# Kernel optimization log

Hardware: AMD Instinct MI355X
Metric: run time of the kernel (lower is better)

The kernel has to match this reference:

```python
import jax, jax.numpy as jnp
import numpy as np

B, C, L = 4, 192, 4096
DIV = 3
CO = C // DIV  # 64


def setup_inputs() -> dict:
    key = jax.random.key(0)
    ks = jax.random.split(key, 6)
    # kaiming-normal-ish init for 1x1 conv weights, stored as (out, in) matrices
    std = float(np.sqrt(2.0 / C))
    return {
        "x": jax.random.normal(ks[0], (B, C, L, 1), dtype=jnp.float32),
        "Wq": jax.random.normal(ks[1], (CO, C), dtype=jnp.float32) * std,
        "Wk": jax.random.normal(ks[2], (CO, C), dtype=jnp.float32) * std,
        "Wv": jax.random.normal(ks[3], (CO, C), dtype=jnp.float32) * std,
        "Wv1": jax.random.normal(ks[4], (CO, C), dtype=jnp.float32) * std,
        "gamma": jnp.zeros((1,), dtype=jnp.float32) + 0.5,  # nonzero so attn path is exercised
    }


def reference(x, Wq, Wk, Wv, Wv1, gamma):
    b, c, l, _ = x.shape
    xf = x.reshape(b, c, l)                      # (B, C, L)
    f = jnp.einsum("oc,bcl->bol", Wq, xf)        # (B, CO, L)
    g = jnp.einsum("oc,bcl->bol", Wk, xf)
    h = jnp.einsum("oc,bcl->bol", Wv, xf)
    v1 = jnp.einsum("oc,bcl->bol", Wv1, xf)
    # scores[b, l, m] = sum_o f[b,o,l] * g[b,o,m]; softmax over dim=1 (l axis)
    scores = jnp.einsum("bol,bom->blm", f, g)    # (B, L, L)
    beta = jax.nn.softmax(scores, axis=1)
    o = gamma * jnp.einsum("bol,blm->bom", h, beta) + v1  # (B, CO, L)
    return o.reshape(b, c // 3, l, 1)
```

## Files before the change

### kernel.cpp

```cpp
#include <hip/hip_runtime.h>
#include <math.h>

#define B_ 4
#define C_ 192
#define L_ 4096
#define CO_ 64
#define LOG2E 1.44269504088896340736f

using half8 = __attribute__((ext_vector_type(8))) _Float16;
using half4v = __attribute__((ext_vector_type(4))) _Float16;
using half2v = __attribute__((ext_vector_type(2))) _Float16;
using f32x16 = __attribute__((ext_vector_type(16))) float;

#if __has_builtin(__builtin_amdgcn_exp2f)
#define EXP2(x) __builtin_amdgcn_exp2f(x)
#else
#define EXP2(x) exp2f(x)
#endif

__device__ inline half2v pkrtz(float a, float b) {
  return __builtin_bit_cast(half2v, __builtin_amdgcn_cvt_pkrtz(a, b));
}


__global__ __launch_bounds__(256) void wpack_kernel(
    const float* __restrict__ Wq, const float* __restrict__ Wk,
    const float* __restrict__ Wv, const float* __restrict__ Wv1,
    _Float16* __restrict__ Wpack) {
  const int tid = blockIdx.x * 256 + threadIdx.x;
  const int w = tid / 1536;
  const int rem = tid % 1536;
  const int og = rem / 768;
  const int ks = (rem % 768) / 64;
  const int lane = rem % 64;
  const float* src = (w == 0) ? Wq : (w == 1) ? Wk : (w == 2) ? Wv : Wv1;
  const float s = (w == 0) ? LOG2E : 1.0f;
  const int row = og * 32 + (lane & 31);
  const int col = ks * 16 + (lane >> 5) * 8;
  const float* p = src + row * C_ + col;
  const float4 a = *(const float4*)(p);
  const float4 c = *(const float4*)(p + 4);
  half8 o;
  half2v t;
  t = pkrtz(a.x * s, a.y * s); o[0] = t[0]; o[1] = t[1];
  t = pkrtz(a.z * s, a.w * s); o[2] = t[0]; o[3] = t[1];
  t = pkrtz(c.x * s, c.y * s); o[4] = t[0]; o[5] = t[1];
  t = pkrtz(c.z * s, c.w * s); o[6] = t[0]; o[7] = t[1];
  *(half8*)(Wpack + (size_t)tid * 8) = o;
}

__global__ __launch_bounds__(256) void proj_mfma(
    const float* __restrict__ x, const _Float16* __restrict__ Wpack,
    _Float16* __restrict__ fPack, _Float16* __restrict__ gPack,
    _Float16* __restrict__ hPack, float* __restrict__ v1N) {
  __shared__ __align__(16) _Float16 xT[32][200];
  __shared__ __align__(16) _Float16 fl[32 * 72];
  __shared__ __align__(16) _Float16 gl[32 * 72];
  __shared__ __align__(16) _Float16 hl[64 * 40];
  __shared__ float vl[64][33];
  const int b = blockIdx.y, T = blockIdx.x, l0 = T * 32;
  const int t = threadIdx.x;
  const int lane = t & 63, w = t >> 6;
  const int m = lane & 31, hi = lane >> 5;
  const int lr = lane & 31, rp = lane >> 5;

  const _Float16* Wp = Wpack + (size_t)w * 1536 * 8;
  half8 wf[2][12];
#pragma unroll
  for (int og = 0; og < 2; ++og)
#pragma unroll
    for (int ks = 0; ks < 12; ++ks)
      wf[og][ks] =
          *(const half8*)(Wp + ((size_t)(og * 12 + ks) * 64 + lane) * 8);

  {
    const float* xb = x + (size_t)b * C_ * L_ + l0 + lr;
    const int c0 = w * 48;
#pragma unroll
    for (int i = 0; i < 24; ++i) {
      const int c = c0 + 2 * i + rp;
      xT[lr][c] = (_Float16)xb[(size_t)c * L_];
    }
  }
  __syncthreads();

  half8 aF[12];
#pragma unroll
  for (int ks = 0; ks < 12; ++ks)
    aF[ks] = *(const half8*)&xT[m][ks * 16 + hi * 8];

  f32x16 acc0 = {}, acc1 = {};
#pragma unroll
  for (int ks = 0; ks < 12; ++ks) {
    acc0 = __builtin_amdgcn_mfma_f32_32x32x16_f16(aF[ks], wf[0][ks], acc0, 0, 0, 0);
    acc1 = __builtin_amdgcn_mfma_f32_32x32x16_f16(aF[ks], wf[1][ks], acc1, 0, 0, 0);
  }

  if (w < 2) {
    _Float16* buf = (w == 0) ? fl : gl;
#pragma unroll
    for (int r = 0; r < 16; ++r) {
      const int l = 4 * hi + 8 * (r >> 2) + (r & 3);
      buf[l * 72 + m] = (_Float16)acc0[r];
      buf[l * 72 + 32 + m] = (_Float16)acc1[r];
    }
    _Float16* dst = ((w == 0) ? fPack : gPack) +
                    (size_t)b * L_ * CO_ + (size_t)T * 4 * 64 * 8;
#pragma unroll
    for (int ks = 0; ks < 4; ++ks) {
      const half8 v =
          *(const half8*)&buf[(lane & 31) * 72 + ks * 16 + (lane >> 5) * 8];
      *(half8*)(dst + ((size_t)ks * 64 + lane) * 8) = v;
    }
  } else if (w == 2) {
#pragma unroll
    for (int r = 0; r < 16; ++r) {
      const int l = 4 * hi + 8 * (r >> 2) + (r & 3);
      hl[m * 40 + l] = (_Float16)acc0[r];
      hl[(32 + m) * 40 + l] = (_Float16)acc1[r];
    }
    _Float16* dst = hPack + (size_t)b * L_ * CO_ + (size_t)T * 4 * 64 * 8;
#pragma unroll
    for (int j = 0; j < 4; ++j) {
      const int oh2 = j >> 1, ks2 = j & 1;
      const half8 v = *(const half8*)&hl[(32 * oh2 + (lane & 31)) * 40 +
                                         ks2 * 16 + (lane >> 5) * 8];
      *(half8*)(dst + ((size_t)j * 64 + lane) * 8) = v;
    }
  } else {
#pragma unroll
    for (int r = 0; r < 16; ++r) {
      const int l = 4 * hi + 8 * (r >> 2) + (r & 3);
      vl[m][l] = acc0[r];
      vl[32 + m][l] = acc1[r];
    }
#pragma unroll
    for (int i = 0; i < 32; ++i) {
      const int o = 2 * i + rp;
      v1N[((size_t)b * CO_ + o) * L_ + l0 + lr] = vl[o][lr];
    }
  }
}

__global__ __launch_bounds__(512, 2) void attn_mfma(
    const _Float16* __restrict__ fPack, const _Float16* __restrict__ gPack,
    const _Float16* __restrict__ hPack, const float* __restrict__ v1N,
    const float* __restrict__ gamma_p, float* __restrict__ out) {
  __shared__ __align__(16) _Float16 Pl[8][64 * 40];
  __shared__ float obuf4[4][CO_][65];
  __shared__ float redM[8][64];
  __shared__ float redZ[8][64];

  const int id = blockIdx.x;
  const int b = (id >> 1) & 3;
  const int mt = ((id & 1) << 5) | (id >> 3);
  const int m0 = mt * 64;
  const int t = threadIdx.x;
  const int lane = t & 63, s = t >> 6;
  const int m = lane & 31, hi = lane >> 5;

  const _Float16* fT = fPack + (size_t)b * L_ * CO_;
  const _Float16* hT = hPack + (size_t)b * L_ * CO_;
  _Float16* Pw = &Pl[s][0];

  half8 gf0[4], gf1[4];
  {
    const _Float16* gp = gPack + (size_t)b * L_ * CO_ +
                         (size_t)(2 * mt) * 4 * 64 * 8 + lane * 8;
#pragma unroll
    for (int ks = 0; ks < 4; ++ks) {
      gf0[ks] = *(const half8*)(gp + (size_t)ks * 64 * 8);
      gf1[ks] = *(const half8*)(gp + (size_t)(4 + ks) * 64 * 8);
    }
  }

  f32x16 o0 = {}, o1 = {}, o2 = {}, o3 = {};
  float mx0 = -1e30f, Z0 = 0.f, mx1 = -1e30f, Z1 = 0.f;

  const int T0 = s * 16;
  half8 fc[2][4];
  f32x16 Sv0[2], Sv1[2];

  {
    const _Float16* fp = fT + ((size_t)T0 * 4 * 64 + lane) * 8;
#pragma unroll
    for (int ks = 0; ks < 4; ++ks)
      fc[0][ks] = *(const half8*)(fp + (size_t)ks * 64 * 8);
    f32x16 z = {};
    Sv0[0] = z; Sv1[0] = z;
#pragma unroll
    for (int ks = 0; ks < 4; ++ks) {
      Sv0[0] = __builtin_amdgcn_mfma_f32_32x32x16_f16(fc[0][ks], gf0[ks], Sv0[0], 0, 0, 0);
      Sv1[0] = __builtin_amdgcn_mfma_f32_32x32x16_f16(fc[0][ks], gf1[ks], Sv1[0], 0, 0, 0);
    }
    const _Float16* fp1 = fT + ((size_t)(T0 + 1) * 4 * 64 + lane) * 8;
#pragma unroll
    for (int ks = 0; ks < 4; ++ks)
      fc[1][ks] = *(const half8*)(fp1 + (size_t)ks * 64 * 8);
  }

#pragma unroll 2
  for (int stp = 0; stp < 16; ++stp) {
    const int cur = stp & 1, nxt = cur ^ 1;
    half8 hc[4];
    {
      const _Float16* hp = hT + ((size_t)(T0 + stp) * 4 * 64 + lane) * 8;
#pragma unroll
      for (int ks = 0; ks < 4; ++ks)
        hc[ks] = *(const half8*)(hp + (size_t)ks * 64 * 8);
    }
    {
      f32x16 z = {};
      Sv0[nxt] = z; Sv1[nxt] = z;
#pragma unroll
      for (int ks = 0; ks < 4; ++ks) {
        Sv0[nxt] = __builtin_amdgcn_mfma_f32_32x32x16_f16(fc[nxt][ks], gf0[ks], Sv0[nxt], 0, 0, 0);
        Sv1[nxt] = __builtin_amdgcn_mfma_f32_32x32x16_f16(fc[nxt][ks], gf1[ks], Sv1[nxt], 0, 0, 0);
      }
    }
    {
      const _Float16* fp = fT + ((size_t)(T0 + stp + 2) * 4 * 64 + lane) * 8;
#pragma unroll
      for (int ks = 0; ks < 4; ++ks)
        fc[cur][ks] = *(const half8*)(fp + (size_t)ks * 64 * 8);
    }
    const f32x16 S0 = Sv0[cur], S1 = Sv1[cur];
    float t0 = S0[0], t1 = S1[0];
#pragma unroll
    for (int r = 1; r < 16; ++r) {
      t0 = fmaxf(t0, S0[r]);
      t1 = fmaxf(t1, S1[r]);
    }
    t0 = fmaxf(t0, __shfl_xor(t0, 32, 64));
    t1 = fmaxf(t1, __shfl_xor(t1, 32, 64));
    if (__any(t0 > mx0 || t1 > mx1)) {
      const float mn0 = fmaxf(mx0, t0), mn1 = fmaxf(mx1, t1);
      const float c0 = EXP2(mx0 - mn0), c1 = EXP2(mx1 - mn1);
      mx0 = mn0; mx1 = mn1;
      Z0 *= c0; Z1 *= c1;
#pragma unroll
      for (int r = 0; r < 16; ++r) {
        o0[r] *= c0; o1[r] *= c0;
        o2[r] *= c1; o3[r] *= c1;
      }
    }
    float zl0 = 0.f, zl1 = 0.f;
#pragma unroll
    for (int u = 0; u < 4; ++u) {
      const float a0 = EXP2(S0[4 * u + 0] - mx0);
      const float a1 = EXP2(S0[4 * u + 1] - mx0);
      const float a2 = EXP2(S0[4 * u + 2] - mx0);
      const float a3 = EXP2(S0[4 * u + 3] - mx0);
      zl0 += (a0 + a1) + (a2 + a3);
      const half2v lo = pkrtz(a0, a1);
      const half2v hi2 = pkrtz(a2, a3);
      half4v w4; w4[0] = lo[0]; w4[1] = lo[1]; w4[2] = hi2[0]; w4[3] = hi2[1];
      *(half4v*)(Pw + m * 40 + 4 * hi + 8 * u) = w4;
      const float b0 = EXP2(S1[4 * u + 0] - mx1);
      const float b1 = EXP2(S1[4 * u + 1] - mx1);
      const float b2 = EXP2(S1[4 * u + 2] - mx1);
      const float b3 = EXP2(S1[4 * u + 3] - mx1);
      zl1 += (b0 + b1) + (b2 + b3);
      const half2v lo2 = pkrtz(b0, b1);
      const half2v hi3 = pkrtz(b2, b3);
      half4v w5; w5[0] = lo2[0]; w5[1] = lo2[1]; w5[2] = hi3[0]; w5[3] = hi3[1];
      *(half4v*)(Pw + (32 + m) * 40 + 4 * hi + 8 * u) = w5;
    }
    Z0 += zl0; Z1 += zl1;
    const half8 bP0 = *(const half8*)(Pw + m * 40 + 8 * hi);
    const half8 bP1 = *(const half8*)(Pw + m * 40 + 16 + 8 * hi);
    const half8 bQ0 = *(const half8*)(Pw + (32 + m) * 40 + 8 * hi);
    const half8 bQ1 = *(const half8*)(Pw + (32 + m) * 40 + 16 + 8 * hi);
    o0 = __builtin_amdgcn_mfma_f32_32x32x16_f16(hc[0], bP0, o0, 0, 0, 0);
    o1 = __builtin_amdgcn_mfma_f32_32x32x16_f16(hc[2], bP0, o1, 0, 0, 0);
    o2 = __builtin_amdgcn_mfma_f32_32x32x16_f16(hc[0], bQ0, o2, 0, 0, 0);
    o3 = __builtin_amdgcn_mfma_f32_32x32x16_f16(hc[2], bQ0, o3, 0, 0, 0);
    o0 = __builtin_amdgcn_mfma_f32_32x32x16_f16(hc[1], bP1, o0, 0, 0, 0);
    o1 = __builtin_amdgcn_mfma_f32_32x32x16_f16(hc[3], bP1, o1, 0, 0, 0);
    o2 = __builtin_amdgcn_mfma_f32_32x32x16_f16(hc[1], bQ1, o2, 0, 0, 0);
    o3 = __builtin_amdgcn_mfma_f32_32x32x16_f16(hc[3], bQ1, o3, 0, 0, 0);
  }

  Z0 += __shfl_xor(Z0, 32, 64);
  Z1 += __shfl_xor(Z1, 32, 64);
  if (hi == 0) {
    redM[s][m] = mx0; redM[s][m + 32] = mx1;
    redZ[s][m] = Z0;  redZ[s][m + 32] = Z1;
  }
  __syncthreads();
  float M0 = redM[0][m], M1 = redM[0][m + 32];
#pragma unroll
  for (int i = 1; i < 8; ++i) {
    M0 = fmaxf(M0, redM[i][m]);
    M1 = fmaxf(M1, redM[i][m + 32]);
  }
  const float sc0 = EXP2(mx0 - M0);
  const float sc1 = EXP2(mx1 - M1);
  if (s < 4) {
#pragma unroll
    for (int r = 0; r < 16; ++r) {
      const int o = 4 * hi + 8 * (r >> 2) + (r & 3);
      obuf4[s][o][m] = sc0 * o0[r];
      obuf4[s][o + 32][m] = sc0 * o1[r];
      obuf4[s][o][m + 32] = sc1 * o2[r];
      obuf4[s][o + 32][m + 32] = sc1 * o3[r];
    }
  }
  __syncthreads();
  if (s >= 4) {
#pragma unroll
    for (int r = 0; r < 16; ++r) {
      const int o = 4 * hi + 8 * (r >> 2) + (r & 3);
      obuf4[s - 4][o][m] += sc0 * o0[r];
      obuf4[s - 4][o + 32][m] += sc0 * o1[r];
      obuf4[s - 4][o][m + 32] += sc1 * o2[r];
      obuf4[s - 4][o + 32][m + 32] += sc1 * o3[r];
    }
  }
  __syncthreads();

  const float gam = gamma_p[0];
  const int me = t & 63;
  const int og = t >> 6;
  float M = redM[0][me];
#pragma unroll
  for (int i = 1; i < 8; ++i) M = fmaxf(M, redM[i][me]);
  float Zt = 0.f;
#pragma unroll
  for (int i = 0; i < 8; ++i) Zt += EXP2(redM[i][me] - M) * redZ[i][me];
  const float inv = 1.0f / Zt;
#pragma unroll
  for (int i = 0; i < 8; ++i) {
    const int o = og * 8 + i;
    const float val = obuf4[0][o][me] + obuf4[1][o][me] +
                      obuf4[2][o][me] + obuf4[3][o][me];
    const size_t g = ((size_t)b * CO_ + o) * L_ + m0 + me;
    out[g] = gam * val * inv + v1N[g];
  }
}

extern "C" void kernel_launch(void* const* d_in, const int* in_sizes, int n_in,
                              void* d_out, int out_size, void* d_ws,
                              size_t ws_size, hipStream_t stream) {
  const float* x = (const float*)d_in[0];
  const float* Wq = (const float*)d_in[1];
  const float* Wk = (const float*)d_in[2];
  const float* Wv = (const float*)d_in[3];
  const float* Wv1 = (const float*)d_in[4];
  const float* gamma = (const float*)d_in[5];
  float* out = (float*)d_out;

  _Float16* Wpack = (_Float16*)d_ws;
  _Float16* fPack = Wpack + (size_t)4 * 1536 * 8;
  _Float16* gPack = fPack + (size_t)B_ * L_ * CO_;
  _Float16* hPack = gPack + (size_t)B_ * L_ * CO_;
  float* v1N = (float*)(hPack + (size_t)B_ * L_ * CO_);

  wpack_kernel<<<24, 256, 0, stream>>>(Wq, Wk, Wv, Wv1, Wpack);
  proj_mfma<<<dim3(L_ / 32, B_), 256, 0, stream>>>(x, Wpack, fPack, gPack,
                                                   hPack, v1N);
  attn_mfma<<<256, 512, 0, stream>>>(fPack, gPack, hPack, v1N, gamma, out);
}
```

Before: 105.1 us.

## Compute softmax denominator via MFMA with ones and restructure f/h prefetch

After: 107.4 us. 1.02x slower.

```diff
diff --git a/kernel.cpp b/kernel.cpp
--- a/kernel.cpp
+++ b/kernel.cpp
@@ -174,57 +174,45 @@
     }
   }
 
+  half8 ones8;
+#pragma unroll
+  for (int e = 0; e < 8; ++e) ones8[e] = (_Float16)1.0f;
+
   f32x16 o0 = {}, o1 = {}, o2 = {}, o3 = {};
-  float mx0 = -1e30f, Z0 = 0.f, mx1 = -1e30f, Z1 = 0.f;
+  f32x16 oz0 = {}, oz1 = {};
+  float mx0 = -1e30f, mx1 = -1e30f;
 
   const int T0 = s * 16;
-  half8 fc[2][4];
-  f32x16 Sv0[2], Sv1[2];
-
+  half8 fc[2][4], hc[2][4];
   {
     const _Float16* fp = fT + ((size_t)T0 * 4 * 64 + lane) * 8;
-#pragma unroll
-    for (int ks = 0; ks < 4; ++ks)
+    const _Float16* hp = hT + ((size_t)T0 * 4 * 64 + lane) * 8;
+#pragma unroll
+    for (int ks = 0; ks < 4; ++ks) {
       fc[0][ks] = *(const half8*)(fp + (size_t)ks * 64 * 8);
-    f32x16 z = {};
-    Sv0[0] = z; Sv1[0] = z;
-#pragma unroll
-    for (int ks = 0; ks < 4; ++ks) {
-      Sv0[0] = __builtin_amdgcn_mfma_f32_32x32x16_f16(fc[0][ks], gf0[ks], Sv0[0], 0, 0, 0);
-      Sv1[0] = __builtin_amdgcn_mfma_f32_32x32x16_f16(fc[0][ks], gf1[ks], Sv1[0], 0, 0, 0);
-    }
-    const _Float16* fp1 = fT + ((size_t)(T0 + 1) * 4 * 64 + lane) * 8;
-#pragma unroll
-    for (int ks = 0; ks < 4; ++ks)
-      fc[1][ks] = *(const half8*)(fp1 + (size_t)ks * 64 * 8);
+      hc[0][ks] = *(const half8*)(hp + (size_t)ks * 64 * 8);
+    }
   }
 
 #pragma unroll 2
   for (int stp = 0; stp < 16; ++stp) {
     const int cur = stp & 1, nxt = cur ^ 1;
-    half8 hc[4];
     {
-      const _Float16* hp = hT + ((size_t)(T0 + stp) * 4 * 64 + lane) * 8;
-#pragma unroll
-      for (int ks = 0; ks < 4; ++ks)
-        hc[ks] = *(const half8*)(hp + (size_t)ks * 64 * 8);
-    }
-    {
-      f32x16 z = {};
-      Sv0[nxt] = z; Sv1[nxt] = z;
+      const int Tn = T0 + stp + 1;
+      const _Float16* fp = fT + ((size_t)Tn * 4 * 64 + lane) * 8;
+      const _Float16* hp = hT + ((size_t)Tn * 4 * 64 + lane) * 8;
 #pragma unroll
       for (int ks = 0; ks < 4; ++ks) {
-        Sv0[nxt] = __builtin_amdgcn_mfma_f32_32x32x16_f16(fc[nxt][ks], gf0[ks], Sv0[nxt], 0, 0, 0);
-        Sv1[nxt] = __builtin_amdgcn_mfma_f32_32x32x16_f16(fc[nxt][ks], gf1[ks], Sv1[nxt], 0, 0, 0);
+        fc[nxt][ks] = *(const half8*)(fp + (size_t)ks * 64 * 8);
+        hc[nxt][ks] = *(const half8*)(hp + (size_t)ks * 64 * 8);
       }
     }
-    {
-      const _Float16* fp = fT + ((size_t)(T0 + stp + 2) * 4 * 64 + lane) * 8;
-#pragma unroll
-      for (int ks = 0; ks < 4; ++ks)
-        fc[cur][ks] = *(const half8*)(fp + (size_t)ks * 64 * 8);
-    }
-    const f32x16 S0 = Sv0[cur], S1 = Sv1[cur];
+    f32x16 S0 = {}, S1 = {};
+#pragma unroll
+    for (int ks = 0; ks < 4; ++ks) {
+      S0 = __builtin_amdgcn_mfma_f32_32x32x16_f16(fc[cur][ks], gf0[ks], S0, 0, 0, 0);
+      S1 = __builtin_amdgcn_mfma_f32_32x32x16_f16(fc[cur][ks], gf1[ks], S1, 0, 0, 0);
+    }
     float t0 = S0[0], t1 = S1[0];
 #pragma unroll
     for (int r = 1; r < 16; ++r) {
@@ -237,21 +225,18 @@
       const float mn0 = fmaxf(mx0, t0), mn1 = fmaxf(mx1, t1);
       const float c0 = EXP2(mx0 - mn0), c1 = EXP2(mx1 - mn1);
       mx0 = mn0; mx1 = mn1;
-      Z0 *= c0; Z1 *= c1;
 #pragma unroll
       for (int r = 0; r < 16; ++r) {
-        o0[r] *= c0; o1[r] *= c0;
-        o2[r] *= c1; o3[r] *= c1;
+        o0[r] *= c0; o1[r] *= c0; oz0[r] *= c0;
+        o2[r] *= c1; o3[r] *= c1; oz1[r] *= c1;
       }
     }
-    float zl0 = 0.f, zl1 = 0.f;
 #pragma unroll
     for (int u = 0; u < 4; ++u) {
       const float a0 = EXP2(S0[4 * u + 0] - mx0);
       const float a1 = EXP2(S0[4 * u + 1] - mx0);
       const float a2 = EXP2(S0[4 * u + 2] - mx0);
       const float a3 = EXP2(S0[4 * u + 3] - mx0);
-      zl0 += (a0 + a1) + (a2 + a3);
       const half2v lo = pkrtz(a0, a1);
       const half2v hi2 = pkrtz(a2, a3);
       half4v w4; w4[0] = lo[0]; w4[1] = lo[1]; w4[2] = hi2[0]; w4[3] = hi2[1];
@@ -260,29 +245,31 @@
       const float b1 = EXP2(S1[4 * u + 1] - mx1);
       const float b2 = EXP2(S1[4 * u + 2] - mx1);
       const float b3 = EXP2(S1[4 * u + 3] - mx1);
-      zl1 += (b0 + b1) + (b2 + b3);
       const half2v lo2 = pkrtz(b0, b1);
       const half2v hi3 = pkrtz(b2, b3);
       half4v w5; w5[0] = lo2[0]; w5[1] = lo2[1]; w5[2] = hi3[0]; w5[3] = hi3[1];
       *(half4v*)(Pw + (32 + m) * 40 + 4 * hi + 8 * u) = w5;
     }
-    Z0 += zl0; Z1 += zl1;
     const half8 bP0 = *(const half8*)(Pw + m * 40 + 8 * hi);
     const half8 bP1 = *(const half8*)(Pw + m * 40 + 16 + 8 * hi);
     const half8 bQ0 = *(const half8*)(Pw + (32 + m) * 40 + 8 * hi);
     const half8 bQ1 = *(const half8*)(Pw + (32 + m) * 40 + 16 + 8 * hi);
-    o0 = __builtin_amdgcn_mfma_f32_32x32x16_f16(hc[0], bP0, o0, 0, 0, 0);
-    o1 = __builtin_amdgcn_mfma_f32_32x32x16_f16(hc[2], bP0, o1, 0, 0, 0);
-    o2 = __builtin_amdgcn_mfma_f32_32x32x16_f16(hc[0], bQ0, o2, 0, 0, 0);
-    o3 = __builtin_amdgcn_mfma_f32_32x32x16_f16(hc[2], bQ0, o3, 0, 0, 0);
-    o0 = __builtin_amdgcn_mfma_f32_32x32x16_f16(hc[1], bP1, o0, 0, 0, 0);
-    o1 = __builtin_amdgcn_mfma_f32_32x32x16_f16(hc[3], bP1, o1, 0, 0, 0);
-    o2 = __builtin_amdgcn_mfma_f32_32x32x16_f16(hc[1], bQ1, o2, 0, 0, 0);
-    o3 = __builtin_amdgcn_mfma_f32_32x32x16_f16(hc[3], bQ1, o3, 0, 0, 0);
-  }
-
-  Z0 += __shfl_xor(Z0, 32, 64);
-  Z1 += __shfl_xor(Z1, 32, 64);
+    o0 = __builtin_amdgcn_mfma_f32_32x32x16_f16(hc[cur][0], bP0, o0, 0, 0, 0);
+    o1 = __builtin_amdgcn_mfma_f32_32x32x16_f16(hc[cur][2], bP0, o1, 0, 0, 0);
+    o2 = __builtin_amdgcn_mfma_f32_32x32x16_f16(hc[cur][0], bQ0, o2, 0, 0, 0);
+    o3 = __builtin_amdgcn_mfma_f32_32x32x16_f16(hc[cur][2], bQ0, o3, 0, 0, 0);
+    oz0 = __builtin_amdgcn_mfma_f32_32x32x16_f16(ones8, bP0, oz0, 0, 0, 0);
+    oz1 = __builtin_amdgcn_mfma_f32_32x32x16_f16(ones8, bQ0, oz1, 0, 0, 0);
+    o0 = __builtin_amdgcn_mfma_f32_32x32x16_f16(hc[cur][1], bP1, o0, 0, 0, 0);
+    o1 = __builtin_amdgcn_mfma_f32_32x32x16_f16(hc[cur][3], bP1, o1, 0, 0, 0);
+    o2 = __builtin_amdgcn_mfma_f32_32x32x16_f16(hc[cur][1], bQ1, o2, 0, 0, 0);
+    o3 = __builtin_amdgcn_mfma_f32_32x32x16_f16(hc[cur][3], bQ1, o3, 0, 0, 0);
+    oz0 = __builtin_amdgcn_mfma_f32_32x32x16_f16(ones8, bP1, oz0, 0, 0, 0);
+    oz1 = __builtin_amdgcn_mfma_f32_32x32x16_f16(ones8, bQ1, oz1, 0, 0, 0);
+  }
+
+  const float Z0 = oz0[0];
+  const float Z1 = oz1[0];
   if (hi == 0) {
     redM[s][m] = mx0; redM[s][m + 32] = mx1;
     redZ[s][m] = Z0;  redZ[s][m + 32] = Z1;
```

## Double attention block waves to 16 and shrink per-wave P buffer

Applied to the files above, without the earlier changes.

Measured after the change: 142.1 us. 1.35x slower.

```diff
diff --git a/kernel.cpp b/kernel.cpp
--- a/kernel.cpp
+++ b/kernel.cpp
@@ -142,14 +142,15 @@
   }
 }
 
-__global__ __launch_bounds__(512, 2) void attn_mfma(
+__global__ __launch_bounds__(1024, 4) void attn_mfma(
     const _Float16* __restrict__ fPack, const _Float16* __restrict__ gPack,
     const _Float16* __restrict__ hPack, const float* __restrict__ v1N,
     const float* __restrict__ gamma_p, float* __restrict__ out) {
-  __shared__ __align__(16) _Float16 Pl[8][64 * 40];
-  __shared__ float obuf4[4][CO_][65];
-  __shared__ float redM[8][64];
-  __shared__ float redZ[8][64];
+  __shared__ __align__(16) char smemRaw[4 * 64 * 65 * 4];
+  __shared__ float redM[16][64];
+  __shared__ float redZ[16][64];
+  _Float16* Pall = (_Float16*)smemRaw;
+  float(*obuf4)[CO_][65] = (float(*)[CO_][65])smemRaw;
 
   const int id = blockIdx.x;
   const int b = (id >> 1) & 3;
@@ -161,7 +162,7 @@
 
   const _Float16* fT = fPack + (size_t)b * L_ * CO_;
   const _Float16* hT = hPack + (size_t)b * L_ * CO_;
-  _Float16* Pw = &Pl[s][0];
+  _Float16* Pw = Pall + s * 32 * 40;
 
   half8 gf0[4], gf1[4];
   {
@@ -177,54 +178,21 @@
   f32x16 o0 = {}, o1 = {}, o2 = {}, o3 = {};
   float mx0 = -1e30f, Z0 = 0.f, mx1 = -1e30f, Z1 = 0.f;
 
-  const int T0 = s * 16;
-  half8 fc[2][4];
-  f32x16 Sv0[2], Sv1[2];
-
-  {
-    const _Float16* fp = fT + ((size_t)T0 * 4 * 64 + lane) * 8;
-#pragma unroll
-    for (int ks = 0; ks < 4; ++ks)
-      fc[0][ks] = *(const half8*)(fp + (size_t)ks * 64 * 8);
-    f32x16 z = {};
-    Sv0[0] = z; Sv1[0] = z;
+  for (int stp = 0; stp < 8; ++stp) {
+    const int Tn = s * 8 + stp;
+    half8 fc[4];
+    {
+      const _Float16* fp = fT + ((size_t)Tn * 4 * 64 + lane) * 8;
+#pragma unroll
+      for (int ks = 0; ks < 4; ++ks)
+        fc[ks] = *(const half8*)(fp + (size_t)ks * 64 * 8);
+    }
+    f32x16 S0 = {}, S1 = {};
 #pragma unroll
     for (int ks = 0; ks < 4; ++ks) {
-      Sv0[0] = __builtin_amdgcn_mfma_f32_32x32x16_f16(fc[0][ks], gf0[ks], Sv0[0], 0, 0, 0);
-      Sv1[0] = __builtin_amdgcn_mfma_f32_32x32x16_f16(fc[0][ks], gf1[ks], Sv1[0], 0, 0, 0);
-    }
-    const _Float16* fp1 = fT + ((size_t)(T0 + 1) * 4 * 64 + lane) * 8;
-#pragma unroll
-    for (int ks = 0; ks < 4; ++ks)
-      fc[1][ks] = *(const half8*)(fp1 + (size_t)ks * 64 * 8);
-  }
-
-#pragma unroll 2
-  for (int stp = 0; stp < 16; ++stp) {
-    const int cur = stp & 1, nxt = cur ^ 1;
-    half8 hc[4];
-    {
-      const _Float16* hp = hT + ((size_t)(T0 + stp) * 4 * 64 + lane) * 8;
-#pragma unroll
-      for (int ks = 0; ks < 4; ++ks)
-        hc[ks] = *(const half8*)(hp + (size_t)ks * 64 * 8);
-    }
-    {
-      f32x16 z = {};
-      Sv0[nxt] = z; Sv1[nxt] = z;
-#pragma unroll
-      for (int ks = 0; ks < 4; ++ks) {
-        Sv0[nxt] = __builtin_amdgcn_mfma_f32_32x32x16_f16(fc[nxt][ks], gf0[ks], Sv0[nxt], 0, 0, 0);
-        Sv1[nxt] = __builtin_amdgcn_mfma_f32_32x32x16_f16(fc[nxt][ks], gf1[ks], Sv1[nxt], 0, 0, 0);
-      }
-    }
-    {
-      const _Float16* fp = fT + ((size_t)(T0 + stp + 2) * 4 * 64 + lane) * 8;
-#pragma unroll
-      for (int ks = 0; ks < 4; ++ks)
-        fc[cur][ks] = *(const half8*)(fp + (size_t)ks * 64 * 8);
-    }
-    const f32x16 S0 = Sv0[cur], S1 = Sv1[cur];
+      S0 = __builtin_amdgcn_mfma_f32_32x32x16_f16(fc[ks], gf0[ks], S0, 0, 0, 0);
+      S1 = __builtin_amdgcn_mfma_f32_32x32x16_f16(fc[ks], gf1[ks], S1, 0, 0, 0);
+    }
     float t0 = S0[0], t1 = S1[0];
 #pragma unroll
     for (int r = 1; r < 16; ++r) {
@@ -234,9 +202,9 @@
     t0 = fmaxf(t0, __shfl_xor(t0, 32, 64));
     t1 = fmaxf(t1, __shfl_xor(t1, 32, 64));
     if (__any(t0 > mx0 || t1 > mx1)) {
-      const float mn0 = fmaxf(mx0, t0), mn1 = fmaxf(mx1, t1);
-      const float c0 = EXP2(mx0 - mn0), c1 = EXP2(mx1 - mn1);
-      mx0 = mn0; mx1 = mn1;
+      const float c0 = EXP2(mx0 - fmaxf(mx0, t0));
+      const float c1 = EXP2(mx1 - fmaxf(mx1, t1));
+      mx0 = fmaxf(mx0, t0); mx1 = fmaxf(mx1, t1);
       Z0 *= c0; Z1 *= c1;
 #pragma unroll
       for (int r = 0; r < 16; ++r) {
@@ -244,41 +212,57 @@
         o2[r] *= c1; o3[r] *= c1;
       }
     }
-    float zl0 = 0.f, zl1 = 0.f;
-#pragma unroll
-    for (int u = 0; u < 4; ++u) {
-      const float a0 = EXP2(S0[4 * u + 0] - mx0);
-      const float a1 = EXP2(S0[4 * u + 1] - mx0);
-      const float a2 = EXP2(S0[4 * u + 2] - mx0);
-      const float a3 = EXP2(S0[4 * u + 3] - mx0);
-      zl0 += (a0 + a1) + (a2 + a3);
-      const half2v lo = pkrtz(a0, a1);
-      const half2v hi2 = pkrtz(a2, a3);
-      half4v w4; w4[0] = lo[0]; w4[1] = lo[1]; w4[2] = hi2[0]; w4[3] = hi2[1];
-      *(half4v*)(Pw + m * 40 + 4 * hi + 8 * u) = w4;
-      const float b0 = EXP2(S1[4 * u + 0] - mx1);
-      const float b1 = EXP2(S1[4 * u + 1] - mx1);
-      const float b2 = EXP2(S1[4 * u + 2] - mx1);
-      const float b3 = EXP2(S1[4 * u + 3] - mx1);
-      zl1 += (b0 + b1) + (b2 + b3);
-      const half2v lo2 = pkrtz(b0, b1);
-      const half2v hi3 = pkrtz(b2, b3);
-      half4v w5; w5[0] = lo2[0]; w5[1] = lo2[1]; w5[2] = hi3[0]; w5[3] = hi3[1];
-      *(half4v*)(Pw + (32 + m) * 40 + 4 * hi + 8 * u) = w5;
-    }
-    Z0 += zl0; Z1 += zl1;
-    const half8 bP0 = *(const half8*)(Pw + m * 40 + 8 * hi);
-    const half8 bP1 = *(const half8*)(Pw + m * 40 + 16 + 8 * hi);
-    const half8 bQ0 = *(const half8*)(Pw + (32 + m) * 40 + 8 * hi);
-    const half8 bQ1 = *(const half8*)(Pw + (32 + m) * 40 + 16 + 8 * hi);
-    o0 = __builtin_amdgcn_mfma_f32_32x32x16_f16(hc[0], bP0, o0, 0, 0, 0);
-    o1 = __builtin_amdgcn_mfma_f32_32x32x16_f16(hc[2], bP0, o1, 0, 0, 0);
-    o2 = __builtin_amdgcn_mfma_f32_32x32x16_f16(hc[0], bQ0, o2, 0, 0, 0);
-    o3 = __builtin_amdgcn_mfma_f32_32x32x16_f16(hc[2], bQ0, o3, 0, 0, 0);
-    o0 = __builtin_amdgcn_mfma_f32_32x32x16_f16(hc[1], bP1, o0, 0, 0, 0);
-    o1 = __builtin_amdgcn_mfma_f32_32x32x16_f16(hc[3], bP1, o1, 0, 0, 0);
-    o2 = __builtin_amdgcn_mfma_f32_32x32x16_f16(hc[1], bQ1, o2, 0, 0, 0);
-    o3 = __builtin_amdgcn_mfma_f32_32x32x16_f16(hc[3], bQ1, o3, 0, 0, 0);
+    half8 hc[4];
+    {
+      const _Float16* hp = hT + ((size_t)Tn * 4 * 64 + lane) * 8;
+#pragma unroll
+      for (int ks = 0; ks < 4; ++ks)
+        hc[ks] = *(const half8*)(hp + (size_t)ks * 64 * 8);
+    }
+    {
+      float zl = 0.f;
+#pragma unroll
+      for (int u = 0; u < 4; ++u) {
+        const float a0 = EXP2(S0[4 * u + 0] - mx0);
+        const float a1 = EXP2(S0[4 * u + 1] - mx0);
+        const float a2 = EXP2(S0[4 * u + 2] - mx0);
+        const float a3 = EXP2(S0[4 * u + 3] - mx0);
+        zl += (a0 + a1) + (a2 + a3);
+        const half2v lo = pkrtz(a0, a1);
+        const half2v hi2 = pkrtz(a2, a3);
+        half4v w4; w4[0] = lo[0]; w4[1] = lo[1]; w4[2] = hi2[0]; w4[3] = hi2[1];
+        *(half4v*)(Pw + m * 40 + 4 * hi + 8 * u) = w4;
+      }
+      Z0 += zl;
+      const half8 bP0 = *(const half8*)(Pw + m * 40 + 8 * hi);
+      const half8 bP1 = *(const half8*)(Pw + m * 40 + 16 + 8 * hi);
+      o0 = __builtin_amdgcn_mfma_f32_32x32x16_f16(hc[0], bP0, o0, 0, 0, 0);
+      o1 = __builtin_amdgcn_mfma_f32_32x32x16_f16(hc[2], bP0, o1, 0, 0, 0);
+      o0 = __builtin_amdgcn_mfma_f32_32x32x16_f16(hc[1], bP1, o0, 0, 0, 0);
+      o1 = __builtin_amdgcn_mfma_f32_32x32x16_f16(hc[3], bP1, o1, 0, 0, 0);
+    }
+    {
+      float zl = 0.f;
+#pragma unroll
+      for (int u = 0; u < 4; ++u) {
+        const float b0 = EXP2(S1[4 * u + 0] - mx1);
+        const float b1 = EXP2(S1[4 * u + 1] - mx1);
+        const float b2 = EXP2(S1[4 * u + 2] - mx1);
+        const float b3 = EXP2(S1[4 * u + 3] - mx1);
+        zl += (b0 + b1) + (b2 + b3);
+        const half2v lo = pkrtz(b0, b1);
+        const half2v hi3 = pkrtz(b2, b3);
+        half4v w5; w5[0] = lo[0]; w5[1] = lo[1]; w5[2] = hi3[0]; w5[3] = hi3[1];
+        *(half4v*)(Pw + m * 40 + 4 * hi + 8 * u) = w5;
+      }
+      Z1 += zl;
+      const half8 bQ0 = *(const half8*)(Pw + m * 40 + 8 * hi);
+      const half8 bQ1 = *(const half8*)(Pw + m * 40 + 16 + 8 * hi);
+      o2 = __builtin_amdgcn_mfma_f32_32x32x16_f16(hc[0], bQ0, o2, 0, 0, 0);
+      o3 = __builtin_amdgcn_mfma_f32_32x32x16_f16(hc[2], bQ0, o3, 0, 0, 0);
+      o2 = __builtin_amdgcn_mfma_f32_32x32x16_f16(hc[1], bQ1, o2, 0, 0, 0);
+      o3 = __builtin_amdgcn_mfma_f32_32x32x16_f16(hc[3], bQ1, o3, 0, 0, 0);
+    }
   }
 
   Z0 += __shfl_xor(Z0, 32, 64);
@@ -290,48 +274,51 @@
   __syncthreads();
   float M0 = redM[0][m], M1 = redM[0][m + 32];
 #pragma unroll
-  for (int i = 1; i < 8; ++i) {
+  for (int i = 1; i < 16; ++i) {
     M0 = fmaxf(M0, redM[i][m]);
     M1 = fmaxf(M1, redM[i][m + 32]);
   }
   const float sc0 = EXP2(mx0 - M0);
   const float sc1 = EXP2(mx1 - M1);
-  if (s < 4) {
-#pragma unroll
-    for (int r = 0; r < 16; ++r) {
-      const int o = 4 * hi + 8 * (r >> 2) + (r & 3);
-      obuf4[s][o][m] = sc0 * o0[r];
-      obuf4[s][o + 32][m] = sc0 * o1[r];
-      obuf4[s][o][m + 32] = sc1 * o2[r];
-      obuf4[s][o + 32][m + 32] = sc1 * o3[r];
-    }
-  }
-  __syncthreads();
-  if (s >= 4) {
-#pragma unroll
-    for (int r = 0; r < 16; ++r) {
-      const int o = 4 * hi + 8 * (r >> 2) + (r & 3);
-      obuf4[s - 4][o][m] += sc0 * o0[r];
-      obuf4[s - 4][o + 32][m] += sc0 * o1[r];
-      obuf4[s - 4][o][m + 32] += sc1 * o2[r];
-      obuf4[s - 4][o + 32][m + 32] += sc1 * o3[r];
-    }
-  }
-  __syncthreads();
+  for (int r0 = 0; r0 < 4; ++r0) {
+    if ((s >> 2) == r0) {
+      const int slot = s & 3;
+      if (r0 == 0) {
+#pragma unroll
+        for (int r = 0; r < 16; ++r) {
+          const int o = 4 * hi + 8 * (r >> 2) + (r & 3);
+          obuf4[slot][o][m] = sc0 * o0[r];
+          obuf4[slot][o + 32][m] = sc0 * o1[r];
+          obuf4[slot][o][m + 32] = sc1 * o2[r];
+          obuf4[slot][o + 32][m + 32] = sc1 * o3[r];
+        }
+      } else {
+#pragma unroll
+        for (int r = 0; r < 16; ++r) {
+          const int o = 4 * hi + 8 * (r >> 2) + (r & 3);
+          obuf4[slot][o][m] += sc0 * o0[r];
+          obuf4[slot][o + 32][m] += sc0 * o1[r];
+          obuf4[slot][o][m + 32] += sc1 * o2[r];
+          obuf4[slot][o + 32][m + 32] += sc1 * o3[r];
+        }
+      }
+    }
+    __syncthreads();
+  }
 
   const float gam = gamma_p[0];
   const int me = t & 63;
   const int og = t >> 6;
   float M = redM[0][me];
 #pragma unroll
-  for (int i = 1; i < 8; ++i) M = fmaxf(M, redM[i][me]);
+  for (int i = 1; i < 16; ++i) M = fmaxf(M, redM[i][me]);
   float Zt = 0.f;
 #pragma unroll
-  for (int i = 0; i < 8; ++i) Zt += EXP2(redM[i][me] - M) * redZ[i][me];
+  for (int i = 0; i < 16; ++i) Zt += EXP2(redM[i][me] - M) * redZ[i][me];
   const float inv = 1.0f / Zt;
 #pragma unroll
-  for (int i = 0; i < 8; ++i) {
-    const int o = og * 8 + i;
+  for (int i = 0; i < 4; ++i) {
+    const int o = og * 4 + i;
     const float val = obuf4[0][o][me] + obuf4[1][o][me] +
                       obuf4[2][o][me] + obuf4[3][o][me];
     const size_t g = ((size_t)b * CO_ + o) * L_ + m0 + me;
@@ -359,5 +346,5 @@
   wpack_kernel<<<24, 256, 0, stream>>>(Wq, Wk, Wv, Wv1, Wpack);
   proj_mfma<<<dim3(L_ / 32, B_), 256, 0, stream>>>(x, Wpack, fPack, gPack,
                                                    hPack, v1N);
-  attn_mfma<<<256, 512, 0, stream>>>(fPack, gPack, hPack, v1N, gamma, out);
-}
+  attn_mfma<<<256, 1024, 0, stream>>>(fPack, gPack, hPack, v1N, gamma, out);
+}
```
